# Performance work log

Measured on AMD Instinct MI355X. Metric: run time of the kernel, lower is better.

Reference implementation:

```python
import jax, jax.numpy as jnp
import numpy as np
from jax import lax

P_BOX, N_PTS, K_MAX, HID, SAMP = 512, 50000, 64, 256, 4
C_IMG, HF, WF = 96, 160, 512
IMG_W, IMG_H = 1280.0, 384.0
OFFSET_SCALE = 0.04
PT_IN = 7


def _lin(key, fan_in, fan_out):
    return jax.random.normal(key, (fan_in, fan_out), dtype=jnp.float32) / np.sqrt(fan_in)


def setup_inputs() -> dict:
    key = jax.random.key(0)
    ks = jax.random.split(key, 24)
    xy = jax.random.uniform(ks[0], (N_PTS, 2), minval=-40.0, maxval=40.0)
    z = jax.random.uniform(ks[1], (N_PTS, 1), minval=-2.0, maxval=4.0)
    feats = jax.random.normal(ks[2], (N_PTS, 4))
    points = jnp.concatenate([xy, z, feats], axis=-1).astype(jnp.float32)
    ctr_xy = jax.random.uniform(ks[3], (P_BOX, 2), minval=-35.0, maxval=35.0)
    ctr_z = jax.random.uniform(ks[4], (P_BOX, 1), minval=-1.0, maxval=2.0)
    dxy = jax.random.uniform(ks[5], (P_BOX, 2), minval=2.0, maxval=6.0)
    dz = jax.random.uniform(ks[6], (P_BOX, 1), minval=1.0, maxval=3.0)
    yaw = jax.random.uniform(ks[7], (P_BOX, 1), minval=-np.pi, maxval=np.pi)
    boxes = jnp.concatenate([ctr_xy, ctr_z, dxy, dz, yaw], axis=-1).astype(jnp.float32)
    image_feat = jax.random.normal(ks[8], (1, C_IMG, HF, WF), dtype=jnp.float32)
    fx = fy = 400.0
    proj = jnp.array([[IMG_W / 2, -fx, 0.0, 0.0], [IMG_H / 2, 0.0, -fy, 0.0], [1.0, 0.0, 0.0, 0.0]], dtype=jnp.float32)
    return {
        'points': points, 'boxes': boxes, 'image_feat': image_feat, 'proj': proj,
        'pe_w1': _lin(ks[9], PT_IN + 1, HID), 'pe_b1': jnp.zeros((HID,), jnp.float32),
        'pe_w2': _lin(ks[10], HID, HID), 'pe_b2': jnp.zeros((HID,), jnp.float32),
        'q_w': _lin(ks[11], HID, HID), 'q_b': jnp.zeros((HID,), jnp.float32),
        'f_w': _lin(ks[12], C_IMG, HID), 'f_b': jnp.zeros((HID,), jnp.float32),
        'off_w': _lin(ks[13], HID, SAMP * 2), 'off_b': jnp.zeros((SAMP * 2,), jnp.float32),
        'wt_w': _lin(ks[14], HID, SAMP), 'wt_b': jnp.zeros((SAMP,), jnp.float32),
        'o_w1': _lin(ks[15], 2 * HID, HID), 'o_b1': jnp.zeros((HID,), jnp.float32),
        'o_w2': _lin(ks[16], HID, HID), 'o_b2': jnp.zeros((HID,), jnp.float32),
        'score_w': _lin(ks[17], HID, 1), 'score_b': jnp.zeros((1,), jnp.float32),
    }


def _fused_features(points, boxes, image_feat, proj, pe_w1, pe_b1, pe_w2, pe_b2,
                    q_w, q_b, f_w, f_b, off_w, off_b, wt_w, wt_b,
                    o_w1, o_b1, o_w2, o_b2, score_w, score_b):
    NEG = jnp.float32(-1e30)
    xyz = points[:, :3]
    ctr, dims, yaw = boxes[:, :3], boxes[:, 3:6], boxes[:, 6]
    c, s = jnp.cos(yaw)[:, None], jnp.sin(yaw)[:, None]
    rel = xyz[None, :, :] - ctr[:, None, :]                      # [P,N,3]
    lx = rel[..., 0] * c + rel[..., 1] * s                       # box-frame coords
    ly = -rel[..., 0] * s + rel[..., 1] * c
    lz = rel[..., 2]
    half = dims[:, None, :] * 0.5
    inside = (jnp.abs(lx) <= half[..., 0]) & (jnp.abs(ly) <= half[..., 1]) & (jnp.abs(lz) <= half[..., 2])
    counts = inside.sum(axis=1)                                  # [P]
    d = jnp.maximum(dims, 1e-3)[:, None, :]
    nx, ny, nz = lx / d[..., 0], ly / d[..., 1], lz / d[..., 2] - 0.5
    planar = jnp.where(inside, jnp.sqrt(nx * nx + ny * ny), jnp.inf)
    _, idx = lax.top_k(-planar, K_MAX)                           # K closest inside points
    slot_valid = jnp.arange(K_MAX)[None, :] < counts[:, None]    # [P,K]
    take = lambda a: jnp.take_along_axis(a, idx, axis=1)
    nl = jnp.stack([take(nx), take(ny), take(nz)], axis=-1)      # [P,K,3]
    nl = jnp.where(slot_valid[..., None], nl, 0.0)
    pts_sel = jnp.where(slot_valid[..., None], points[idx], 0.0)  # [P,K,7]
    # local density: knn(4) mean distance, excluding self
    diff = nl[:, :, None, :] - nl[:, None, :, :]
    dmat = jnp.sqrt((diff * diff).sum(-1) + 1e-12)               # [P,K,K]
    dmat = jnp.where(slot_valid[:, None, :], dmat, jnp.inf)
    knn = -lax.top_k(-dmat, 4)[0]                                # 4 smallest, col0 = self
    m = jnp.minimum(counts, K_MAX)
    col_ok = jnp.arange(1, 4)[None, None, :] < jnp.minimum(m, 4)[:, None, None]
    nb = jnp.where(col_ok, knn[:, :, 1:], 0.0)
    n_nb = jnp.maximum(jnp.minimum(m, 4) - 1, 1).astype(nl.dtype)
    density = jnp.where(slot_valid, jnp.exp(-nb.sum(-1) / n_nb[:, None]), 0.0)  # [P,K]
    tokens = jnp.concatenate([nl, pts_sel[:, :, 3:PT_IN], density[..., None]], axis=-1)  # [P,K,8]
    h = jnp.maximum(tokens @ pe_w1 + pe_b1, 0.0) @ pe_w2 + pe_b2  # point encoder [P,K,H]
    # project points to normalized image coords
    hom = pts_sel[:, :, :3] @ proj[:, :3].T + proj[:, 3]
    depth = hom[..., 2]
    safe_d = jnp.where(jnp.abs(depth) > 1e-3, depth, 1e-3)
    rx = 2.0 * (hom[..., 0] / safe_d) / (IMG_W - 1.0) - 1.0
    ry = 2.0 * (hom[..., 1] / safe_d) / (IMG_H - 1.0) - 1.0
    ref = jnp.stack([rx, ry], axis=-1)                           # [P,K,2]
    valid = (depth > 0.1) & (jnp.abs(rx) <= 1.0) & (jnp.abs(ry) <= 1.0) & slot_valid
    # cross-modal deformable attention (lite)
    q = h @ q_w + q_b
    fm = jnp.einsum('chw,cd->dhw', image_feat[0], f_w) + f_b[:, None, None]  # [H,Hf,Wf]
    offs = (jnp.tanh(h @ off_w + off_b)).reshape(P_BOX, K_MAX, SAMP, 2) * OFFSET_SCALE
    w = jax.nn.softmax(h @ wt_w + wt_b, axis=-1)                 # [P,K,S]
    grid = jnp.clip(ref[:, :, None, :] + offs, -1.2, 1.2)
    px = (grid[..., 0] + 1.0) * 0.5 * (WF - 1)                   # align_corners=True
    py = (grid[..., 1] + 1.0) * 0.5 * (HF - 1)
    x0, y0 = jnp.floor(px), jnp.floor(py)

    def gather(xi, yi):
        inb = (xi >= 0) & (xi <= WF - 1) & (yi >= 0) & (yi <= HF - 1)
        xc = jnp.clip(xi, 0, WF - 1).astype(jnp.int32)
        yc = jnp.clip(yi, 0, HF - 1).astype(jnp.int32)
        return fm[:, yc, xc] * inb[None].astype(fm.dtype)        # [H,P,K,S]

    wx1, wy1 = px - x0, py - y0
    samp = (gather(x0, y0) * (1 - wx1) * (1 - wy1) + gather(x0 + 1, y0) * wx1 * (1 - wy1)
            + gather(x0, y0 + 1) * (1 - wx1) * wy1 + gather(x0 + 1, y0 + 1) * wx1 * wy1)
    samp = jnp.moveaxis(samp, 0, -1)                             # [P,K,S,H]
    vm = valid.astype(h.dtype)
    samp = samp * vm[:, :, None, None]
    w = w * vm[:, :, None]
    w = w / jnp.maximum(w.sum(-1, keepdims=True), 1e-6)
    context = (samp * w[..., None]).sum(axis=2) * vm[..., None]  # [P,K,H]
    cat = jnp.concatenate([q * vm[..., None], context], axis=-1)
    img_tok = jnp.maximum(cat @ o_w1 + o_b1, 0.0) @ o_w2 + o_b2
    fused = h + img_tok                                          # [P,K,H]
    # masked attention pooling over valid slots
    logits = (fused @ score_w + score_b).squeeze(-1)
    logits = jnp.where(slot_valid, logits, NEG)
    valid_rows = slot_valid.any(axis=1)
    logits = jnp.where(valid_rows[:, None], logits, 0.0)
    pw = jnp.where(valid_rows[:, None], jax.nn.softmax(logits, axis=-1), 0.0)
    pooled = jnp.einsum('pk,pkd->pd', pw, fused)                 # [P,H]
    return pooled, counts.astype(jnp.float32)[:, None]


def reference(points, boxes, image_feat, proj, pe_w1, pe_b1, pe_w2, pe_b2,
              q_w, q_b, f_w, f_b, off_w, off_b, wt_w, wt_b,
              o_w1, o_b1, o_w2, o_b2, score_w, score_b):
    return _fused_features(points, boxes, image_feat, proj, pe_w1, pe_b1, pe_w2, pe_b2,
                           q_w, q_b, f_w, f_b, off_w, off_b, wt_w, wt_b,
                           o_w1, o_b1, o_w2, o_b2, score_w, score_b)
```

## Files before the change

kernel.cpp:

```cpp
#include <hip/hip_runtime.h>
#include <hip/hip_bf16.h>

#define P_BOX 512
#define NP    50000
#define NPAD  50176
#define KM    64
#define NKEY  4096
#define HF    160
#define WF    512

typedef unsigned long long u64;
typedef unsigned short u16;
typedef unsigned int u32;
typedef __attribute__((ext_vector_type(8))) short short8;
typedef __attribute__((ext_vector_type(4))) float f32x4;

__device__ __forceinline__ u16 f2bf(float f) {
  u32 u = __float_as_uint(f);
  u32 r = u + 0x7fffu + ((u >> 16) & 1u);
  return (u16)(r >> 16);
}
__device__ __forceinline__ float bf2f(u16 h) { return __uint_as_float(((u32)h) << 16); }
__device__ __forceinline__ float bfl(u32 u) { return __uint_as_float(u << 16); }
__device__ __forceinline__ float bfh(u32 u) { return __uint_as_float(u & 0xffff0000u); }

__device__ __forceinline__ int aIdx(int m, int d) {
  return m * 256 + (((d >> 3) ^ (m & 7)) << 3) + (d & 7);
}
__device__ __forceinline__ const short8* aGr(const u16* A, int m, int g) {
  return (const short8*)(A + m * 256 + ((g ^ (m & 7)) << 3));
}

__launch_bounds__(256)
__global__ void k_prep(const float* __restrict__ pts, const float* __restrict__ img,
                       const float* __restrict__ q_w, const float* __restrict__ q_b,
                       const float* __restrict__ f_w, const float* __restrict__ f_b,
                       const float* __restrict__ o_w1, const float* __restrict__ pe_w1,
                       const float* __restrict__ pe_w2, const float* __restrict__ o_w2,
                       const float* __restrict__ off_w, const float* __restrict__ wt_w,
                       const float* __restrict__ off_b, const float* __restrict__ wt_b,
                       float* __restrict__ xs, float* __restrict__ ys, float* __restrict__ zs,
                       u16* __restrict__ pe_w2T, u16* __restrict__ WqT,
                       u16* __restrict__ o_w2T, u16* __restrict__ FoT,
                       u16* __restrict__ HWT, u16* __restrict__ pe_w1T,
                       float* __restrict__ bq, float* __restrict__ fbo,
                       float* __restrict__ hb, u16* __restrict__ imgT) {
  __shared__ float shbuf[8580];
  const int blk = blockIdx.x;
  const int t = threadIdx.x;

  if (blk < 1280) {
    int w0 = (blk & 7) * 64;
    int h = blk >> 3;
    int c0 = t >> 6, w = t & 63;
    for (int it = 0; it < 24; ++it) {
      int c = it * 4 + c0;
      shbuf[c * 65 + w] = img[(c * HF + h) * WF + w0 + w];
    }
    __syncthreads();
    for (int it = 0; it < 24; ++it) {
      int idx = it * 256 + t;
      int ww = idx / 96, c = idx % 96;
      imgT[((size_t)(h * WF + w0 + ww)) * 96 + c] = f2bf(shbuf[c * 65 + ww]);
    }
  } else if (blk < 1329) {
    int g = blk - 1280;
#pragma unroll
    for (int r = 0; r < 4; ++r) {
      int i = g * 1024 + r * 256 + t;
      if (i < NPAD) {
        if (i < NP) {
          xs[i] = pts[i * 7 + 0];
          ys[i] = pts[i * 7 + 1];
          zs[i] = pts[i * 7 + 2];
        } else {
          xs[i] = 1e9f; ys[i] = 1e9f; zs[i] = 1e9f;
        }
      }
    }
  } else if (blk < 1353) {
    int gg = blk - 1329;
    const bool isWq = gg < 16;
    const int g = isWq ? gg : gg - 16;
    const int n0 = (g & 3) * 64;
    const int x0 = (g >> 2) * 64;
    float* sA = shbuf;
    float* sB = shbuf + 64 * 65;
    float acc[4][4];
#pragma unroll
    for (int r = 0; r < 4; ++r)
#pragma unroll
      for (int c = 0; c < 4; ++c) acc[r][c] = 0.f;
    const int tx = t & 15, ty = t >> 4;
    for (int j0 = 0; j0 < 256; j0 += 64) {
      {
        int nn = t & 63, jb = t >> 6;
#pragma unroll
        for (int r = 0; r < 16; ++r) {
          int jj = jb + r * 4;
          int row = (isWq ? 0 : 256) + j0 + jj;
          sA[jj * 65 + nn] = o_w1[row * 256 + n0 + nn];
        }
      }
      {
        int jj = t & 63, xb = t >> 6;
#pragma unroll
        for (int r = 0; r < 16; ++r) {
          int xx = xb + r * 4;
          float v = 0.f;
          if (isWq) v = q_w[(x0 + xx) * 256 + j0 + jj];
          else if (x0 + xx < 96) v = f_w[(x0 + xx) * 256 + j0 + jj];
          sB[jj * 65 + xx] = v;
        }
      }
      __syncthreads();
#pragma unroll 8
      for (int jj = 0; jj < 64; ++jj) {
        float a[4], b[4];
#pragma unroll
        for (int r = 0; r < 4; ++r) a[r] = sA[jj * 65 + ty * 4 + r];
#pragma unroll
        for (int c = 0; c < 4; ++c) b[c] = sB[jj * 65 + tx * 4 + c];
#pragma unroll
        for (int r = 0; r < 4; ++r)
#pragma unroll
          for (int c = 0; c < 4; ++c) acc[r][c] += a[r] * b[c];
      }
      __syncthreads();
    }
    if (isWq) {
#pragma unroll
      for (int r = 0; r < 4; ++r) {
        ushort4 o;
        o.x = f2bf(acc[r][0]); o.y = f2bf(acc[r][1]);
        o.z = f2bf(acc[r][2]); o.w = f2bf(acc[r][3]);
        *(ushort4*)(WqT + (size_t)(n0 + ty * 4 + r) * 256 + x0 + tx * 4) = o;
      }
    } else if (x0 + tx * 4 < 96) {
#pragma unroll
      for (int r = 0; r < 4; ++r) {
        ushort4 o;
        o.x = f2bf(acc[r][0]); o.y = f2bf(acc[r][1]);
        o.z = f2bf(acc[r][2]); o.w = f2bf(acc[r][3]);
        *(ushort4*)(FoT + (size_t)(n0 + ty * 4 + r) * 96 + x0 + tx * 4) = o;
      }
    }
  } else if (blk < 1385) {
    int g = blk - 1353;
    const float* src = (g < 16) ? pe_w2 : o_w2;
    u16* dst = (g < 16) ? pe_w2T : o_w2T;
    int tile = g & 15;
    int n0 = (tile & 3) * 64, k0 = (tile >> 2) * 64;
    {
      int nn = t & 63, kb = t >> 6;
#pragma unroll
      for (int r = 0; r < 16; ++r) {
        int kk = kb + r * 4;
        shbuf[kk * 65 + nn] = src[(k0 + kk) * 256 + n0 + nn];
      }
    }
    __syncthreads();
    {
      int kk = t & 63, nb = t >> 6;
#pragma unroll
      for (int r = 0; r < 16; ++r) {
        int nn = nb + r * 4;
        dst[(size_t)(n0 + nn) * 256 + k0 + kk] = f2bf(shbuf[kk * 65 + nn]);
      }
    }
  } else {
    int n = t;
    float a1 = 0.f, a2 = 0.f;
    for (int j = 0; j < 256; ++j) {
      a1 += q_b[j] * o_w1[j * 256 + n];
      a2 += f_b[j] * o_w1[(256 + j) * 256 + n];
    }
    bq[n] = a1;
    fbo[n] = a2;
#pragma unroll
    for (int s = 0; s < 16; ++s) {
      float v = (s < 8) ? off_w[n * 8 + s] : ((s < 12) ? wt_w[n * 4 + (s - 8)] : 0.f);
      HWT[s * 256 + n] = f2bf(v);
    }
#pragma unroll
    for (int k = 0; k < 32; ++k)
      pe_w1T[n * 32 + k] = (k < 8) ? f2bf(pe_w1[k * 256 + n]) : (u16)0;
    if (t < 16) hb[t] = (t < 8) ? off_b[t] : ((t < 12) ? wt_b[t - 8] : 0.f);
  }
}

__attribute__((amdgpu_flat_work_group_size(512, 512), amdgpu_waves_per_eu(4, 4)))
__global__ void k_main(const float* __restrict__ pts, const float* __restrict__ boxes,
                       const float* __restrict__ proj,
                       const u16* __restrict__ pe_w1T, const float* __restrict__ pe_b1,
                       const float* __restrict__ pe_b2,
                       const float* __restrict__ o_b1, const float* __restrict__ o_b2,
                       const float* __restrict__ score_w, const float* __restrict__ score_b,
                       const float* __restrict__ xs, const float* __restrict__ ys,
                       const float* __restrict__ zs,
                       const u16* __restrict__ pe_w2T, const u16* __restrict__ WqT,
                       const u16* __restrict__ o_w2T, const u16* __restrict__ FoT,
                       const u16* __restrict__ HWT,
                       const float* __restrict__ bqv, const float* __restrict__ fbov,
                       const float* __restrict__ hbv,
                       const u16* __restrict__ imgT, float* __restrict__ out) {
  __shared__ __align__(16) char smem[81920];
  u16* A1 = (u16*)smem;
  u16* A2 = (u16*)(smem + 32768);
  u16* CTX = (u16*)(smem + 65536);
  float* poolf = (float*)(smem + 65536);
  float* s_nl = poolf;
  float* s_xyz = poolf + 192;
  float* s_ft = poolf + 384;
  u16* s_tokb = (u16*)(poolf + 640);
  float* s_vm = (float*)(smem + 77824);
  float* s_coef = s_vm + 64;
  float* s_wl = s_coef + 64;
  float* s_ref = s_wl + 256;
  float* s_lg = s_ref + 128;
  float* s_pw = s_lg + 64;
  u16* s_offb = (u16*)(s_pw + 64);
  int* cntp = (int*)(s_offb + 512);
  u64* keys = (u64*)smem;
  u64* keys2 = (u64*)(smem + 32768);
  float* s_knn = (float*)(smem + 32768 + 1024);

  const int p = blockIdx.x;
  const int tid = threadIdx.x;

  const float cx = boxes[p * 7 + 0], cy = boxes[p * 7 + 1], cz = boxes[p * 7 + 2];
  const float dx = boxes[p * 7 + 3], dy = boxes[p * 7 + 4], dz = boxes[p * 7 + 5];
  const float yaw = boxes[p * 7 + 6];
  const float cth = cosf(yaw), sth = sinf(yaw);
  const float hx = dx * 0.5f, hy = dy * 0.5f, hz = dz * 0.5f;
  const float ddx = fmaxf(dx, 1e-3f), ddy = fmaxf(dy, 1e-3f), ddz = fmaxf(dz, 1e-3f);

  if (tid == 0) *cntp = 0;
  __syncthreads();

  for (int i = tid * 4; i < NPAD; i += 2048) {
    float4 x4 = *(const float4*)(xs + i);
    float4 y4 = *(const float4*)(ys + i);
    float4 z4 = *(const float4*)(zs + i);
#pragma unroll
    for (int c = 0; c < 4; ++c) {
      float xv = (c == 0) ? x4.x : (c == 1) ? x4.y : (c == 2) ? x4.z : x4.w;
      float yv = (c == 0) ? y4.x : (c == 1) ? y4.y : (c == 2) ? y4.z : y4.w;
      float zv = (c == 0) ? z4.x : (c == 1) ? z4.y : (c == 2) ? z4.z : z4.w;
      float rx0 = xv - cx, ry0 = yv - cy, rz0 = zv - cz;
      float lx = rx0 * cth + ry0 * sth;
      float ly = ry0 * cth - rx0 * sth;
      if (fabsf(lx) <= hx && fabsf(ly) <= hy && fabsf(rz0) <= hz) {
        int pos = atomicAdd(cntp, 1);
        if (pos < NKEY) {
          float nx = lx / ddx, ny = ly / ddy;
          float pl = sqrtf(nx * nx + ny * ny);
          keys[pos] = (((u64)__float_as_uint(pl)) << 32) | (u32)(i + c);
        }
      }
    }
  }
  __syncthreads();
  const int cnt = *cntp;
  const int m = min(cnt, KM);

  if (cnt <= KM) {
    if (tid < cnt) keys2[tid] = keys[tid];
  } else {
    int cc = min(cnt, NKEY);
    if (cc <= 1024) {
      u64 k0v = ~0ull, k1v = ~0ull;
      bool h0 = tid < cc, h1 = tid + 512 < cc;
      if (h0) k0v = keys[tid];
      if (h1) k1v = keys[tid + 512];
      int r0 = 0, r1 = 0;
      for (int i = 0; i < cc; ++i) {
        u64 ki = keys[i];
        r0 += (ki < k0v) ? 1 : 0;
        r1 += (ki < k1v) ? 1 : 0;
      }
      if (h0 && r0 < KM) keys2[r0] = k0v;
      if (h1 && r1 < KM) keys2[r1] = k1v;
    } else {
      int nn = 2048;
      while (nn < cc) nn <<= 1;
      for (int i = cc + tid; i < nn; i += 512) keys[i] = ~0ull;
      __syncthreads();
      for (int k = 2; k <= nn; k <<= 1) {
        for (int j = k >> 1; j > 0; j >>= 1) {
          for (int t = tid; t < nn; t += 512) {
            int ixj = t ^ j;
            if (ixj > t) {
              u64 a = keys[t], b = keys[ixj];
              bool up = ((t & k) == 0);
              if ((a > b) == up) { keys[t] = b; keys[ixj] = a; }
            }
          }
          __syncthreads();
        }
      }
      if (tid < KM) keys2[tid] = keys[tid];
    }
  }
  __syncthreads();

  if (tid < KM) {
    int k = tid;
    float x = 0.f, y = 0.f, z = 0.f, n0 = 0.f, n1 = 0.f, n2 = 0.f;
    float f0 = 0.f, f1 = 0.f, f2 = 0.f, f3 = 0.f;
    if (k < m) {
      u32 pi = (u32)(keys2[k] & 0xffffffffu);
      const float* pp = pts + (size_t)pi * 7;
      x = pp[0]; y = pp[1]; z = pp[2];
      f0 = pp[3]; f1 = pp[4]; f2 = pp[5]; f3 = pp[6];
      float rx0 = x - cx, ry0 = y - cy, rz0 = z - cz;
      float lx = rx0 * cth + ry0 * sth;
      float ly = ry0 * cth - rx0 * sth;
      n0 = lx / ddx; n1 = ly / ddy; n2 = rz0 / ddz - 0.5f;
    }
    s_nl[k * 3 + 0] = n0; s_nl[k * 3 + 1] = n1; s_nl[k * 3 + 2] = n2;
    s_xyz[k * 3 + 0] = x; s_xyz[k * 3 + 1] = y; s_xyz[k * 3 + 2] = z;
    s_ft[k * 4 + 0] = f0; s_ft[k * 4 + 1] = f1; s_ft[k * 4 + 2] = f2; s_ft[k * 4 + 3] = f3;
    float h0 = proj[0] * x + proj[1] * y + proj[2] * z + proj[3];
    float h1 = proj[4] * x + proj[5] * y + proj[6] * z + proj[7];
    float dep = proj[8] * x + proj[9] * y + proj[10] * z + proj[11];
    float sd = (fabsf(dep) > 1e-3f) ? dep : 1e-3f;
    float rx = 2.f * (h0 / sd) / 1279.f - 1.f;
    float ry = 2.f * (h1 / sd) / 383.f - 1.f;
    bool v = (dep > 0.1f) && (fabsf(rx) <= 1.f) && (fabsf(ry) <= 1.f) && (k < m);
    s_vm[k] = v ? 1.f : 0.f;
    s_ref[k * 2 + 0] = rx;
    s_ref[k * 2 + 1] = ry;
  }
  __syncthreads();

  {
    int k = tid & 63, part = tid >> 6;
    float a0 = s_nl[k * 3], a1 = s_nl[k * 3 + 1], a2 = s_nl[k * 3 + 2];
    float b0 = 1e30f, b1 = 1e30f, b2 = 1e30f, b3 = 1e30f;
#pragma unroll
    for (int jj = 0; jj < 8; ++jj) {
      int j = part * 8 + jj;
      if (j < m) {
        float d0 = a0 - s_nl[j * 3], d1 = a1 - s_nl[j * 3 + 1], d2 = a2 - s_nl[j * 3 + 2];
        float dd = sqrtf(d0 * d0 + d1 * d1 + d2 * d2 + 1e-12f);
        if (dd < b3) {
          if (dd < b0)      { b3 = b2; b2 = b1; b1 = b0; b0 = dd; }
          else if (dd < b1) { b3 = b2; b2 = b1; b1 = dd; }
          else if (dd < b2) { b3 = b2; b2 = dd; }
          else              { b3 = dd; }
        }
      }
    }
    float* o = s_knn + k * 32 + part * 4;
    o[0] = b0; o[1] = b1; o[2] = b2; o[3] = b3;
  }
  __syncthreads();

  if (tid < KM) {
    int k = tid;
    float dens = 0.f;
    if (k < m) {
      float b0 = 1e30f, b1 = 1e30f, b2 = 1e30f, b3 = 1e30f;
#pragma unroll
      for (int i = 0; i < 32; ++i) {
        float dd = s_knn[k * 32 + i];
        if (dd < b3) {
          if (dd < b0)      { b3 = b2; b2 = b1; b1 = b0; b0 = dd; }
          else if (dd < b1) { b3 = b2; b2 = b1; b1 = dd; }
          else if (dd < b2) { b3 = b2; b2 = dd; }
          else              { b3 = dd; }
        }
      }
      int mm = min(m, 4);
      float nbs = 0.f;
      if (mm > 1) nbs += b1;
      if (mm > 2) nbs += b2;
      if (mm > 3) nbs += b3;
      dens = expf(-nbs / (float)max(mm - 1, 1));
    }
    u32 w0 = (u32)f2bf(s_nl[k * 3 + 0]) | ((u32)f2bf(s_nl[k * 3 + 1]) << 16);
    u32 w1 = (u32)f2bf(s_nl[k * 3 + 2]) | ((u32)f2bf(s_ft[k * 4 + 0]) << 16);
    u32 w2 = (u32)f2bf(s_ft[k * 4 + 1]) | ((u32)f2bf(s_ft[k * 4 + 2]) << 16);
    u32 w3 = (u32)f2bf(s_ft[k * 4 + 3]) | ((u32)f2bf(dens) << 16);
    uint4* tb = (uint4*)(s_tokb + k * 32);
    tb[0] = make_uint4(w0, w1, w2, w3);
    tb[1] = make_uint4(0, 0, 0, 0);
    tb[2] = make_uint4(0, 0, 0, 0);
    tb[3] = make_uint4(0, 0, 0, 0);
  }
  __syncthreads();

  const int wv = tid >> 6, lane = tid & 63, q = lane >> 4, ln = lane & 15;
  const int n0g = wv * 32;

#pragma unroll
  for (int nt = 0; nt < 2; ++nt) {
    int n = n0g + nt * 16 + ln;
    f32x4 aH[4];
#pragma unroll
    for (int mt = 0; mt < 4; ++mt) aH[mt] = (f32x4)0.f;
    short8 b = *(const short8*)(pe_w1T + (size_t)n * 32 + q * 8);
#pragma unroll
    for (int mt = 0; mt < 4; ++mt) {
      short8 af = *(const short8*)(s_tokb + (ln + 16 * mt) * 32 + q * 8);
      aH[mt] = __builtin_amdgcn_mfma_f32_16x16x32_bf16(af, b, aH[mt], 0, 0, 0);
    }
    float bias = pe_b1[n];
#pragma unroll
    for (int mt = 0; mt < 4; ++mt)
#pragma unroll
      for (int r = 0; r < 4; ++r)
        A1[aIdx(mt * 16 + q * 4 + r, n)] = f2bf(fmaxf(aH[mt][r] + bias, 0.f));
  }
  __syncthreads();

#pragma unroll
  for (int nt = 0; nt < 2; ++nt) {
    int n = n0g + nt * 16 + ln;
    f32x4 acc[4];
#pragma unroll
    for (int mt = 0; mt < 4; ++mt) acc[mt] = (f32x4)0.f;
    const u16* B = pe_w2T + (size_t)n * 256 + q * 8;
#pragma unroll
    for (int ks = 0; ks < 8; ++ks) {
      short8 b = *(const short8*)(B + ks * 32);
#pragma unroll
      for (int mt = 0; mt < 4; ++mt) {
        short8 af = *aGr(A1, ln + 16 * mt, ks * 4 + q);
        acc[mt] = __builtin_amdgcn_mfma_f32_16x16x32_bf16(af, b, acc[mt], 0, 0, 0);
      }
    }
    float bias = pe_b2[n];
#pragma unroll
    for (int mt = 0; mt < 4; ++mt)
#pragma unroll
      for (int r = 0; r < 4; ++r)
        A2[aIdx(mt * 16 + q * 4 + r, n)] = f2bf(acc[mt][r] + bias);
  }
  __syncthreads();

  if (wv < 4) {
    f32x4 acc = (f32x4)0.f;
    const u16* B = HWT + (size_t)ln * 256 + q * 8;
#pragma unroll
    for (int ks = 0; ks < 8; ++ks) {
      short8 af = *aGr(A2, ln + 16 * wv, ks * 4 + q);
      short8 b = *(const short8*)(B + ks * 32);
      acc = __builtin_amdgcn_mfma_f32_16x16x32_bf16(af, b, acc, 0, 0, 0);
    }
    float hb_ = hbv[ln];
#pragma unroll
    for (int r = 0; r < 4; ++r) {
      int mm = wv * 16 + q * 4 + r;
      float val = acc[r] + hb_;
      if (ln < 8) s_offb[mm * 8 + ln] = f2bf(tanhf(val) * 0.04f);
      else if (ln < 12) s_wl[mm * 4 + (ln - 8)] = val;
    }
  }
  __syncthreads();

  if (tid < KM) {
    int k = tid;
    float l0 = s_wl[k * 4], l1 = s_wl[k * 4 + 1], l2 = s_wl[k * 4 + 2], l3 = s_wl[k * 4 + 3];
    float mx = fmaxf(fmaxf(l0, l1), fmaxf(l2, l3));
    float e0 = expf(l0 - mx), e1 = expf(l1 - mx), e2 = expf(l2 - mx), e3 = expf(l3 - mx);
    float si = 1.f / (e0 + e1 + e2 + e3);
    s_wl[k * 4] = e0 * si; s_wl[k * 4 + 1] = e1 * si;
    s_wl[k * 4 + 2] = e2 * si; s_wl[k * 4 + 3] = e3 * si;
  }
  __syncthreads();

  {
    int k = tid >> 3, cg = tid & 7;
    float acc[12];
#pragma unroll
    for (int c = 0; c < 12; ++c) acc[c] = 0.f;
    float coef_ = 0.f;
    if (s_vm[k] > 0.f) {
      float rx = s_ref[k * 2], ry = s_ref[k * 2 + 1];
#pragma unroll
      for (int s = 0; s < 4; ++s) {
        float ox = bf2f(s_offb[k * 8 + s * 2]), oy = bf2f(s_offb[k * 8 + s * 2 + 1]);
        float gx = fminf(fmaxf(rx + ox, -1.2f), 1.2f);
        float gy = fminf(fmaxf(ry + oy, -1.2f), 1.2f);
        float px = (gx + 1.f) * 0.5f * 511.f;
        float py = (gy + 1.f) * 0.5f * 159.f;
        float x0f = floorf(px), y0f = floorf(py);
        float wx1 = px - x0f, wy1 = py - y0f;
        float ws_ = s_wl[k * 4 + s];
        int x0 = (int)x0f, y0 = (int)y0f;
#pragma unroll
        for (int t2 = 0; t2 < 4; ++t2) {
          int xi = x0 + (t2 & 1), yi = y0 + (t2 >> 1);
          if (xi >= 0 && xi <= WF - 1 && yi >= 0 && yi <= HF - 1) {
            float tw = ((t2 & 1) ? wx1 : 1.f - wx1) * ((t2 >> 1) ? wy1 : 1.f - wy1);
            float w2 = ws_ * tw;
            coef_ += w2;
            const u16* pp = imgT + ((size_t)(yi * WF + xi)) * 96 + cg * 12;
            uint2 u0 = *(const uint2*)pp;
            uint2 u1 = *(const uint2*)(pp + 4);
            uint2 u2 = *(const uint2*)(pp + 8);
            acc[0] += w2 * bfl(u0.x); acc[1] += w2 * bfh(u0.x);
            acc[2] += w2 * bfl(u0.y); acc[3] += w2 * bfh(u0.y);
            acc[4] += w2 * bfl(u1.x); acc[5] += w2 * bfh(u1.x);
            acc[6] += w2 * bfl(u1.y); acc[7] += w2 * bfh(u1.y);
            acc[8] += w2 * bfl(u2.x); acc[9] += w2 * bfh(u2.x);
            acc[10] += w2 * bfl(u2.y); acc[11] += w2 * bfh(u2.y);
          }
        }
      }
    }
    u16* cp = CTX + k * 96 + cg * 12;
    u32 o0 = (u32)f2bf(acc[0]) | ((u32)f2bf(acc[1]) << 16);
    u32 o1 = (u32)f2bf(acc[2]) | ((u32)f2bf(acc[3]) << 16);
    u32 o2 = (u32)f2bf(acc[4]) | ((u32)f2bf(acc[5]) << 16);
    u32 o3 = (u32)f2bf(acc[6]) | ((u32)f2bf(acc[7]) << 16);
    u32 o4 = (u32)f2bf(acc[8]) | ((u32)f2bf(acc[9]) << 16);
    u32 o5 = (u32)f2bf(acc[10]) | ((u32)f2bf(acc[11]) << 16);
    *(uint2*)cp = make_uint2(o0, o1);
    *(uint2*)(cp + 4) = make_uint2(o2, o3);
    *(uint2*)(cp + 8) = make_uint2(o4, o5);
    if (cg == 0) s_coef[k] = coef_;
  }
  __syncthreads();

#pragma unroll
  for (int nt = 0; nt < 2; ++nt) {
    int n = n0g + nt * 16 + ln;
    f32x4 aB[4];
#pragma unroll
    for (int mt = 0; mt < 4; ++mt) aB[mt] = (f32x4)0.f;
    const u16* BF = FoT + (size_t)n * 96 + q * 8;
#pragma unroll
    for (int ks = 0; ks < 3; ++ks) {
      short8 b = *(const short8*)(BF + ks * 32);
#pragma unroll
      for (int mt = 0; mt < 4; ++mt) {
        short8 cf = *(const short8*)(CTX + (ln + 16 * mt) * 96 + ks * 32 + q * 8);
        aB[mt] = __builtin_amdgcn_mfma_f32_16x16x32_bf16(cf, b, aB[mt], 0, 0, 0);
      }
    }
    const u16* BW = WqT + (size_t)n * 256 + q * 8;
#pragma unroll
    for (int ks = 0; ks < 8; ++ks) {
      short8 b = *(const short8*)(BW + ks * 32);
#pragma unroll
      for (int mt = 0; mt < 4; ++mt) {
        short8 af = *aGr(A2, ln + 16 * mt, ks * 4 + q);
        aB[mt] = __builtin_amdgcn_mfma_f32_16x16x32_bf16(af, b, aB[mt], 0, 0, 0);
      }
    }
    float fb = fbov[n], ob = o_b1[n], bq_ = bqv[n];
#pragma unroll
    for (int mt = 0; mt < 4; ++mt)
#pragma unroll
      for (int r = 0; r < 4; ++r) {
        int mm = mt * 16 + q * 4 + r;
        float val = (s_vm[mm] > 0.f) ? (aB[mt][r] + bq_ + s_coef[mm] * fb + ob) : ob;
        A1[aIdx(mm, n)] = f2bf(fmaxf(val, 0.f));
      }
  }
  __syncthreads();

#pragma unroll
  for (int nt = 0; nt < 2; ++nt) {
    int n = n0g + nt * 16 + ln;
    f32x4 acc[4];
#pragma unroll
    for (int mt = 0; mt < 4; ++mt) acc[mt] = (f32x4)0.f;
    const u16* B = o_w2T + (size_t)n * 256 + q * 8;
#pragma unroll
    for (int ks = 0; ks < 8; ++ks) {
      short8 b = *(const short8*)(B + ks * 32);
#pragma unroll
      for (int mt = 0; mt < 4; ++mt) {
        short8 af = *aGr(A1, ln + 16 * mt, ks * 4 + q);
        acc[mt] = __builtin_amdgcn_mfma_f32_16x16x32_bf16(af, b, acc[mt], 0, 0, 0);
      }
    }
    float b2 = o_b2[n];
#pragma unroll
    for (int mt = 0; mt < 4; ++mt)
#pragma unroll
      for (int r = 0; r < 4; ++r) {
        int mm = mt * 16 + q * 4 + r;
        int i0 = aIdx(mm, n);
        A2[i0] = f2bf(bf2f(A2[i0]) + acc[mt][r] + b2);
      }
  }
  __syncthreads();

  {
    int k = tid >> 3, part = tid & 7;
    float a = 0.f;
#pragma unroll
    for (int gi = 0; gi < 4; ++gi) {
      int g = part * 4 + gi;
      uint4 uu = *(const uint4*)aGr(A2, k, g);
      const float4* sw = (const float4*)(score_w + g * 8);
      float4 s0 = sw[0], s1 = sw[1];
      a += bfl(uu.x) * s0.x + bfh(uu.x) * s0.y + bfl(uu.y) * s0.z + bfh(uu.y) * s0.w;
      a += bfl(uu.z) * s1.x + bfh(uu.z) * s1.y + bfl(uu.w) * s1.z + bfh(uu.w) * s1.w;
    }
    poolf[k * 8 + part] = a;
  }
  __syncthreads();
  if (tid < KM) {
    float a = score_b[0];
#pragma unroll
    for (int j = 0; j < 8; ++j) a += poolf[tid * 8 + j];
    s_lg[tid] = a;
  }
  __syncthreads();

  if (wv == 0) {
    int k = lane;
    float lg = (k < m) ? s_lg[k] : -1e30f;
    float mx = lg;
#pragma unroll
    for (int o = 32; o; o >>= 1) mx = fmaxf(mx, __shfl_xor(mx, o));
    float e = (k < m) ? expf(lg - mx) : 0.f;
    float ss = e;
#pragma unroll
    for (int o = 32; o; o >>= 1) ss += __shfl_xor(ss, o);
    s_pw[k] = (m > 0 && k < m) ? e / ss : 0.f;
  }
  __syncthreads();

  if (tid < 256) {
    int d = tid;
    float acc = 0.f;
    for (int k = 0; k < KM; ++k) acc += s_pw[k] * bf2f(A2[aIdx(k, d)]);
    out[(size_t)p * 256 + d] = acc;
  }
  if (tid == 0) out[(size_t)P_BOX * 256 + p] = (float)cnt;
}

extern "C" void kernel_launch(void* const* d_in, const int* in_sizes, int n_in,
                              void* d_out, int out_size, void* d_ws, size_t ws_size,
                              hipStream_t stream) {
  (void)in_sizes; (void)n_in; (void)out_size; (void)ws_size;
  const float* points  = (const float*)d_in[0];
  const float* boxes   = (const float*)d_in[1];
  const float* img     = (const float*)d_in[2];
  const float* proj    = (const float*)d_in[3];
  const float* pe_w1   = (const float*)d_in[4];
  const float* pe_b1   = (const float*)d_in[5];
  const float* pe_w2   = (const float*)d_in[6];
  const float* pe_b2   = (const float*)d_in[7];
  const float* q_w     = (const float*)d_in[8];
  const float* q_b     = (const float*)d_in[9];
  const float* f_w     = (const float*)d_in[10];
  const float* f_b     = (const float*)d_in[11];
  const float* off_w   = (const float*)d_in[12];
  const float* off_b   = (const float*)d_in[13];
  const float* wt_w    = (const float*)d_in[14];
  const float* wt_b    = (const float*)d_in[15];
  const float* o_w1    = (const float*)d_in[16];
  const float* o_b1    = (const float*)d_in[17];
  const float* o_w2    = (const float*)d_in[18];
  const float* o_b2    = (const float*)d_in[19];
  const float* score_w = (const float*)d_in[20];
  const float* score_b = (const float*)d_in[21];
  float* out = (float*)d_out;

  char* W = (char*)d_ws;
  float* xs    = (float*)(W + 0);
  float* ysv   = (float*)(W + 200704);
  float* zsv   = (float*)(W + 401408);
  float* bqv   = (float*)(W + 602112);
  float* fbov  = (float*)(W + 603136);
  float* hbv   = (float*)(W + 604160);
  u16* pe_w2T  = (u16*)(W + 604416);
  u16* WqT     = (u16*)(W + 735488);
  u16* o_w2T   = (u16*)(W + 866560);
  u16* FoT     = (u16*)(W + 997632);
  u16* HWT     = (u16*)(W + 1046784);
  u16* pe_w1T  = (u16*)(W + 1054976);
  u16* imgT    = (u16*)(W + 1071360);

  k_prep<<<1386, 256, 0, stream>>>(points, img, q_w, q_b, f_w, f_b, o_w1, pe_w1, pe_w2,
                                   o_w2, off_w, wt_w, off_b, wt_b, xs, ysv, zsv,
                                   pe_w2T, WqT, o_w2T, FoT, HWT, pe_w1T, bqv, fbov, hbv, imgT);
  k_main<<<P_BOX, 512, 0, stream>>>(points, boxes, proj, pe_w1T, pe_b1, pe_b2, o_b1, o_b2,
                                    score_w, score_b, xs, ysv, zsv, pe_w2T, WqT, o_w2T,
                                    FoT, HWT, bqv, fbov, hbv, imgT, out);
}
```

Baseline: 234.4 us.

## Split fused kernel into point-selection kernel and MLP kernel

```diff
diff --git a/kernel.cpp b/kernel.cpp
--- a/kernel.cpp
+++ b/kernel.cpp
@@ -189,41 +189,19 @@
   }
 }
 
-__attribute__((amdgpu_flat_work_group_size(512, 512), amdgpu_waves_per_eu(4, 4)))
-__global__ void k_main(const float* __restrict__ pts, const float* __restrict__ boxes,
-                       const float* __restrict__ proj,
-                       const u16* __restrict__ pe_w1T, const float* __restrict__ pe_b1,
-                       const float* __restrict__ pe_b2,
-                       const float* __restrict__ o_b1, const float* __restrict__ o_b2,
-                       const float* __restrict__ score_w, const float* __restrict__ score_b,
-                       const float* __restrict__ xs, const float* __restrict__ ys,
-                       const float* __restrict__ zs,
-                       const u16* __restrict__ pe_w2T, const u16* __restrict__ WqT,
-                       const u16* __restrict__ o_w2T, const u16* __restrict__ FoT,
-                       const u16* __restrict__ HWT,
-                       const float* __restrict__ bqv, const float* __restrict__ fbov,
-                       const float* __restrict__ hbv,
-                       const u16* __restrict__ imgT, float* __restrict__ out) {
-  __shared__ __align__(16) char smem[81920];
-  u16* A1 = (u16*)smem;
-  u16* A2 = (u16*)(smem + 32768);
-  u16* CTX = (u16*)(smem + 65536);
-  float* poolf = (float*)(smem + 65536);
-  float* s_nl = poolf;
-  float* s_xyz = poolf + 192;
-  float* s_ft = poolf + 384;
-  u16* s_tokb = (u16*)(poolf + 640);
-  float* s_vm = (float*)(smem + 77824);
-  float* s_coef = s_vm + 64;
-  float* s_wl = s_coef + 64;
-  float* s_ref = s_wl + 256;
-  float* s_lg = s_ref + 128;
-  float* s_pw = s_lg + 64;
-  u16* s_offb = (u16*)(s_pw + 64);
-  int* cntp = (int*)(s_offb + 512);
-  u64* keys = (u64*)smem;
-  u64* keys2 = (u64*)(smem + 32768);
-  float* s_knn = (float*)(smem + 32768 + 1024);
+__launch_bounds__(512)
+__global__ void k_sel(const float* __restrict__ pts, const float* __restrict__ boxes,
+                      const float* __restrict__ proj,
+                      const float* __restrict__ xs, const float* __restrict__ ys,
+                      const float* __restrict__ zs,
+                      uint4* __restrict__ TOK, float* __restrict__ VM,
+                      float* __restrict__ REF, int* __restrict__ CNT,
+                      float* __restrict__ out) {
+  __shared__ u64 keys[NKEY];
+  __shared__ u64 keys2[KM];
+  __shared__ float s_nl[KM * 3], s_ft[KM * 4];
+  __shared__ float s_knn[KM * 32];
+  __shared__ int cntp;
 
   const int p = blockIdx.x;
   const int tid = threadIdx.x;
@@ -235,7 +213,7 @@
   const float hx = dx * 0.5f, hy = dy * 0.5f, hz = dz * 0.5f;
   const float ddx = fmaxf(dx, 1e-3f), ddy = fmaxf(dy, 1e-3f), ddz = fmaxf(dz, 1e-3f);
 
-  if (tid == 0) *cntp = 0;
+  if (tid == 0) cntp = 0;
   __syncthreads();
 
   for (int i = tid * 4; i < NPAD; i += 2048) {
@@ -251,7 +229,7 @@
       float lx = rx0 * cth + ry0 * sth;
       float ly = ry0 * cth - rx0 * sth;
       if (fabsf(lx) <= hx && fabsf(ly) <= hy && fabsf(rz0) <= hz) {
-        int pos = atomicAdd(cntp, 1);
+        int pos = atomicAdd(&cntp, 1);
         if (pos < NKEY) {
           float nx = lx / ddx, ny = ly / ddy;
           float pl = sqrtf(nx * nx + ny * ny);
@@ -261,7 +239,7 @@
     }
   }
   __syncthreads();
-  const int cnt = *cntp;
+  const int cnt = cntp;
   const int m = min(cnt, KM);
 
   if (cnt <= KM) {
@@ -319,7 +297,6 @@
       n0 = lx / ddx; n1 = ly / ddy; n2 = rz0 / ddz - 0.5f;
     }
     s_nl[k * 3 + 0] = n0; s_nl[k * 3 + 1] = n1; s_nl[k * 3 + 2] = n2;
-    s_xyz[k * 3 + 0] = x; s_xyz[k * 3 + 1] = y; s_xyz[k * 3 + 2] = z;
     s_ft[k * 4 + 0] = f0; s_ft[k * 4 + 1] = f1; s_ft[k * 4 + 2] = f2; s_ft[k * 4 + 3] = f3;
     float h0 = proj[0] * x + proj[1] * y + proj[2] * z + proj[3];
     float h1 = proj[4] * x + proj[5] * y + proj[6] * z + proj[7];
@@ -328,9 +305,9 @@
     float rx = 2.f * (h0 / sd) / 1279.f - 1.f;
     float ry = 2.f * (h1 / sd) / 383.f - 1.f;
     bool v = (dep > 0.1f) && (fabsf(rx) <= 1.f) && (fabsf(ry) <= 1.f) && (k < m);
-    s_vm[k] = v ? 1.f : 0.f;
-    s_ref[k * 2 + 0] = rx;
-    s_ref[k * 2 + 1] = ry;
+    VM[p * KM + k] = v ? 1.f : 0.f;
+    REF[p * KM * 2 + k * 2 + 0] = rx;
+    REF[p * KM * 2 + k * 2 + 1] = ry;
   }
   __syncthreads();
 
@@ -383,11 +360,57 @@
     u32 w1 = (u32)f2bf(s_nl[k * 3 + 2]) | ((u32)f2bf(s_ft[k * 4 + 0]) << 16);
     u32 w2 = (u32)f2bf(s_ft[k * 4 + 1]) | ((u32)f2bf(s_ft[k * 4 + 2]) << 16);
     u32 w3 = (u32)f2bf(s_ft[k * 4 + 3]) | ((u32)f2bf(dens) << 16);
+    TOK[p * KM + k] = make_uint4(w0, w1, w2, w3);
+  }
+  if (tid == 0) {
+    CNT[p] = cnt;
+    out[(size_t)P_BOX * 256 + p] = (float)cnt;
+  }
+}
+
+__attribute__((amdgpu_flat_work_group_size(512, 512), amdgpu_waves_per_eu(4, 4)))
+__global__ void k_mlp(const u16* __restrict__ pe_w1T, const float* __restrict__ pe_b1,
+                      const float* __restrict__ pe_b2,
+                      const float* __restrict__ o_b1, const float* __restrict__ o_b2,
+                      const float* __restrict__ score_w, const float* __restrict__ score_b,
+                      const u16* __restrict__ pe_w2T, const u16* __restrict__ WqT,
+                      const u16* __restrict__ o_w2T, const u16* __restrict__ FoT,
+                      const u16* __restrict__ HWT,
+                      const float* __restrict__ bqv, const float* __restrict__ fbov,
+                      const float* __restrict__ hbv,
+                      const u16* __restrict__ imgT,
+                      const uint4* __restrict__ TOK, const float* __restrict__ VM,
+                      const float* __restrict__ REF, const int* __restrict__ CNT,
+                      float* __restrict__ out) {
+  __shared__ __align__(16) char smem[81920];
+  u16* A1 = (u16*)smem;
+  u16* A2 = (u16*)(smem + 32768);
+  u16* CTX = (u16*)(smem + 65536);
+  float* poolf = (float*)(smem + 65536);
+  u16* s_tokb = (u16*)(poolf + 640);
+  float* s_vm = (float*)(smem + 77824);
+  float* s_coef = s_vm + 64;
+  float* s_wl = s_coef + 64;
+  float* s_ref = s_wl + 256;
+  float* s_lg = s_ref + 128;
+  float* s_pw = s_lg + 64;
+  u16* s_offb = (u16*)(s_pw + 64);
+
+  const int p = blockIdx.x;
+  const int tid = threadIdx.x;
+  const int m = min(CNT[p], KM);
+
+  if (tid < KM) {
+    int k = tid;
+    uint4 tv = TOK[p * KM + k];
     uint4* tb = (uint4*)(s_tokb + k * 32);
-    tb[0] = make_uint4(w0, w1, w2, w3);
+    tb[0] = tv;
     tb[1] = make_uint4(0, 0, 0, 0);
     tb[2] = make_uint4(0, 0, 0, 0);
     tb[3] = make_uint4(0, 0, 0, 0);
+    s_vm[k] = VM[p * KM + k];
+    s_ref[k * 2 + 0] = REF[p * KM * 2 + k * 2 + 0];
+    s_ref[k * 2 + 1] = REF[p * KM * 2 + k * 2 + 1];
   }
   __syncthreads();
 
@@ -634,7 +657,6 @@
     for (int k = 0; k < KM; ++k) acc += s_pw[k] * bf2f(A2[aIdx(k, d)]);
     out[(size_t)p * 256 + d] = acc;
   }
-  if (tid == 0) out[(size_t)P_BOX * 256 + p] = (float)cnt;
 }
 
 extern "C" void kernel_launch(void* const* d_in, const int* in_sizes, int n_in,
@@ -679,11 +701,17 @@
   u16* HWT     = (u16*)(W + 1046784);
   u16* pe_w1T  = (u16*)(W + 1054976);
   u16* imgT    = (u16*)(W + 1071360);
+  uint4* TOK   = (uint4*)(W + 16800000);
+  float* VM    = (float*)(W + 17324288);
+  float* REF   = (float*)(W + 17455360);
+  int*   CNTW  = (int*)(W + 17717504);
 
   k_prep<<<1386, 256, 0, stream>>>(points, img, q_w, q_b, f_w, f_b, o_w1, pe_w1, pe_w2,
                                    o_w2, off_w, wt_w, off_b, wt_b, xs, ysv, zsv,
                                    pe_w2T, WqT, o_w2T, FoT, HWT, pe_w1T, bqv, fbov, hbv, imgT);
-  k_main<<<P_BOX, 512, 0, stream>>>(points, boxes, proj, pe_w1T, pe_b1, pe_b2, o_b1, o_b2,
-                                    score_w, score_b, xs, ysv, zsv, pe_w2T, WqT, o_w2T,
-                                    FoT, HWT, bqv, fbov, hbv, imgT, out);
+  k_sel<<<P_BOX, 512, 0, stream>>>(points, boxes, proj, xs, ysv, zsv,
+                                   TOK, VM, REF, CNTW, out);
+  k_mlp<<<P_BOX, 512, 0, stream>>>(pe_w1T, pe_b1, pe_b2, o_b1, o_b2, score_w, score_b,
+                                   pe_w2T, WqT, o_w2T, FoT, HWT, bqv, fbov, hbv, imgT,
+                                   TOK, VM, REF, CNTW, out);
 }
```

Result: slower. 239.6 us (+2.2%).
